# Kernel optimization log

Measured on AMD Instinct MI355X. Metric: run time of the kernel, lower is better.

## Reference

```python
import jax, jax.numpy as jnp
import numpy as np

NUM_HEADS = 16
KEY_DIM = 64
B, S, D = 2, 2048, 1024


def setup_inputs() -> dict:
    key = jax.random.key(0)
    ks = jax.random.split(key, 5)
    scale = 1.0 / np.sqrt(D)
    return {
        "x": jax.random.normal(ks[0], (B, S, D), dtype=jnp.float32),
        "Wq": jax.random.normal(ks[1], (D, NUM_HEADS * KEY_DIM), dtype=jnp.float32) * scale,
        "Wk": jax.random.normal(ks[2], (D, NUM_HEADS * KEY_DIM), dtype=jnp.float32) * scale,
        "Wv": jax.random.normal(ks[3], (D, NUM_HEADS * KEY_DIM), dtype=jnp.float32) * scale,
        "Wo": jax.random.normal(ks[4], (NUM_HEADS * KEY_DIM, D), dtype=jnp.float32) * scale,
    }


def reference(x, Wq, Wk, Wv, Wo):
    b, s, d = x.shape
    h, kd = NUM_HEADS, KEY_DIM
    # QKV projections -> [B, H, S, Kd]
    q = (x @ Wq).reshape(b, s, h, kd).transpose(0, 2, 1, 3)
    k = (x @ Wk).reshape(b, s, h, kd).transpose(0, 2, 1, 3)
    v = (x @ Wv).reshape(b, s, h, kd).transpose(0, 2, 1, 3)
    # scaled dot-product attention, full [B,H,S,S] scores (faithful to source)
    logits = jnp.einsum("bhqd,bhkd->bhqk", q, k) / jnp.sqrt(jnp.float32(kd))
    attn = jax.nn.softmax(logits, axis=-1)
    out = jnp.einsum("bhqk,bhkd->bhqd", attn, v)  # [B,H,S,Kd]
    out = out.transpose(0, 2, 1, 3).reshape(b, s, h * kd)
    return out @ Wo
```

## Files before the change

kernel.cpp:

```cpp
#include <hip/hip_runtime.h>


typedef __attribute__((ext_vector_type(8))) short short8;
typedef __attribute__((ext_vector_type(4))) float f32x4;

#define M_ROWS 4096
#define N_COLS 1024
#define K_DIM  1024
#define SEQ    2048

#define QSCALE 0.18033688011111772f

#if defined(__has_builtin)
#if __has_builtin(__builtin_amdgcn_exp2f)
#define EXP2(x) __builtin_amdgcn_exp2f(x)
#endif
#endif
#ifndef EXP2
#define EXP2(x) exp2f(x)
#endif

#define WAITCNT_VM8 0x0F78

__device__ inline unsigned short f2bf(float f) {
  unsigned int u = __float_as_uint(f);
  u += 0x7fffu + ((u >> 16) & 1u);
  return (unsigned short)(u >> 16);
}

__device__ inline unsigned int pack2bf(float a, float b) {
  unsigned int ua = __float_as_uint(a); ua += 0x7fffu + ((ua >> 16) & 1u);
  unsigned int ub = __float_as_uint(b); ub += 0x7fffu + ((ub >> 16) & 1u);
  return (ua >> 16) | (ub & 0xffff0000u);
}

__device__ inline void async_load16(const unsigned short* gptr, unsigned short* lptr) {
  __builtin_amdgcn_global_load_lds(
      (const __attribute__((address_space(1))) unsigned int*)gptr,
      (__attribute__((address_space(3))) unsigned int*)lptr, 16, 0, 0);
}

__global__ void detect_kernel(const unsigned short* __restrict__ x, int* __restrict__ flag) {
  __shared__ int bad;
  if (threadIdx.x == 0) bad = 0;
  __syncthreads();
  for (int i = threadIdx.x; i < 1024; i += 256) {
    float f = __uint_as_float((unsigned int)x[i] << 16);
    float a = fabsf(f);
    if (!(a < 1e4f)) atomicOr(&bad, 1);
  }
  __syncthreads();
  if (threadIdx.x == 0) *flag = bad ? 0 : 1;
}

__global__ void convert_kernel(const void* __restrict__ src, unsigned short* __restrict__ dst,
                               int n4, const int* __restrict__ flag) {
  const int isbf = *flag;
  const int stride = gridDim.x * blockDim.x;
  for (int i = blockIdx.x * blockDim.x + threadIdx.x; i < n4; i += stride) {
    if (isbf) {
      ((uint2*)dst)[i] = ((const uint2*)src)[i];
    } else {
      float4 v = ((const float4*)src)[i];
      ushort4 o;
      o.x = f2bf(v.x); o.y = f2bf(v.y); o.z = f2bf(v.z); o.w = f2bf(v.w);
      ((ushort4*)dst)[i] = o;
    }
  }
}

__global__ __launch_bounds__(256) void convert_wT4_kernel(
    const void* __restrict__ s0, const void* __restrict__ s1,
    const void* __restrict__ s2, const void* __restrict__ s3,
    unsigned short* __restrict__ d0, unsigned short* __restrict__ d1,
    unsigned short* __restrict__ d2, unsigned short* __restrict__ d3,
    const int* __restrict__ flag) {
  __shared__ unsigned short t[32][33];
  const int z = blockIdx.z;
  const void* src = (z == 0) ? s0 : (z == 1) ? s1 : (z == 2) ? s2 : s3;
  unsigned short* dst = (z == 0) ? d0 : (z == 1) ? d1 : (z == 2) ? d2 : d3;
  const int tid = threadIdx.x;
  const int r0 = blockIdx.y * 32, c0 = blockIdx.x * 32;
  const int kr = tid >> 3, nc = (tid & 7) * 4;
  if (*flag) {
    const unsigned short* W = (const unsigned short*)src;
    uint2 v = *(const uint2*)(W + (size_t)(r0 + kr) * K_DIM + c0 + nc);
    t[kr][nc] = v.x & 0xffff; t[kr][nc + 1] = v.x >> 16;
    t[kr][nc + 2] = v.y & 0xffff; t[kr][nc + 3] = v.y >> 16;
  } else {
    const float* W = (const float*)src;
    float4 v = *(const float4*)(W + (size_t)(r0 + kr) * K_DIM + c0 + nc);
    t[kr][nc] = f2bf(v.x); t[kr][nc + 1] = f2bf(v.y);
    t[kr][nc + 2] = f2bf(v.z); t[kr][nc + 3] = f2bf(v.w);
  }
  __syncthreads();
  const int nr = tid >> 3, kc = (tid & 7) * 4;
  uint2 w;
  w.x = (unsigned int)t[kc][nr] | ((unsigned int)t[kc + 1][nr] << 16);
  w.y = (unsigned int)t[kc + 2][nr] | ((unsigned int)t[kc + 3][nr] << 16);
  *(uint2*)(dst + (size_t)(c0 + nr) * K_DIM + r0 + kc) = w;
}

#define GEMM_MAIN_LOOP(Aptr, Bptr, KTOT)                                          \
  f32x4 acc[4][4];                                                                \
  _Pragma("unroll") for (int i = 0; i < 4; ++i)                                   \
  _Pragma("unroll") for (int j = 0; j < 4; ++j)                                   \
      acc[i][j] = (f32x4){0.f, 0.f, 0.f, 0.f};                                    \
  for (int kb = 0; kb < (KTOT); kb += 64) {                                       \
    _Pragma("unroll") for (int r = 0; r < 4; ++r) {                               \
      int s = r * 256 + wave * 64 + lane;                                         \
      int row = s >> 3, c = s & 7;                                                \
      int g = c ^ (row & 7);                                                      \
      async_load16((Aptr) + (size_t)(m0 + row) * (KTOT) + kb + g * 8,             \
                   &As[(size_t)(r * 256 + wave * 64) * 8]);                       \
      async_load16((Bptr) + (size_t)(n0 + row) * (KTOT) + kb + g * 8,             \
                   &Bs[(size_t)(r * 256 + wave * 64) * 8]);                       \
    }                                                                             \
    __syncthreads();                                                              \
    _Pragma("unroll") for (int h = 0; h < 2; ++h) {                               \
      short8 am[4], bn[4];                                                        \
      _Pragma("unroll") for (int i = 0; i < 4; ++i) {                             \
        int row = wr * 64 + i * 16 + l15;                                         \
        int cc = (h * 4 + quad) ^ (row & 7);                                      \
        am[i] = *(const short8*)(&As[row * 64 + cc * 8]);                         \
      }                                                                           \
      _Pragma("unroll") for (int j = 0; j < 4; ++j) {                             \
        int row = wc * 64 + j * 16 + l15;                                         \
        int cc = (h * 4 + quad) ^ (row & 7);                                      \
        bn[j] = *(const short8*)(&Bs[row * 64 + cc * 8]);                         \
      }                                                                           \
      _Pragma("unroll") for (int i = 0; i < 4; ++i)                               \
      _Pragma("unroll") for (int j = 0; j < 4; ++j)                               \
          acc[i][j] = __builtin_amdgcn_mfma_f32_16x16x32_bf16(am[i], bn[j],       \
                                                              acc[i][j], 0, 0, 0);\
    }                                                                             \
    __syncthreads();                                                              \
  }

__global__ __launch_bounds__(256) void qkv_gemm_kernel(
    const unsigned short* __restrict__ Xb,
    const unsigned short* __restrict__ Wqt,
    const unsigned short* __restrict__ Wkt,
    const unsigned short* __restrict__ Wvt,
    unsigned short* __restrict__ Qb,
    unsigned short* __restrict__ Kb,
    unsigned short* __restrict__ Vt) {
  __shared__ __align__(16) unsigned short As[128 * 64];
  __shared__ __align__(16) unsigned short Bs[128 * 64];
  const int tid = threadIdx.x;
  const int wave = tid >> 6, lane = tid & 63;
  const int quad = lane >> 4, l15 = lane & 15;
  const int wr = wave >> 1, wc = wave & 1;
  const int m0 = blockIdx.x * 128;
  const int n0 = blockIdx.y * 128;
  const int wsel = blockIdx.z;
  const unsigned short* __restrict__ Bt =
      (wsel == 0) ? Wqt : ((wsel == 1) ? Wkt : Wvt);

  GEMM_MAIN_LOOP(Xb, Bt, K_DIM)

#pragma unroll
  for (int i = 0; i < 4; ++i) {
#pragma unroll
    for (int j = 0; j < 4; ++j) {
      int mbase = m0 + wr * 64 + i * 16 + quad * 4;
      int n = n0 + wc * 64 + j * 16 + l15;
      int h = n >> 6, d = n & 63;
      if (wsel == 2) {
        int b_ = mbase >> 11, s = mbase & 2047;
        uint2 w;
        w.x = pack2bf(acc[i][j][0], acc[i][j][1]);
        w.y = pack2bf(acc[i][j][2], acc[i][j][3]);
        *(uint2*)(Vt + ((size_t)(b_ * 16 + h) * 64 + d) * SEQ + s) = w;
      } else {
#pragma unroll
        for (int r = 0; r < 4; ++r) {
          int m = mbase + r;
          int b_ = m >> 11, s = m & 2047;
          float val = acc[i][j][r];
          if (wsel == 0)
            Qb[((size_t)(b_ * 16 + h) * SEQ + s) * 64 + d] = f2bf(val * QSCALE);
          else
            Kb[((size_t)(b_ * 16 + h) * SEQ + s) * 64 + d] = f2bf(val);
        }
      }
    }
  }
}

__global__ __launch_bounds__(256, 2) void flash_kernel(
    const unsigned short* __restrict__ Qb,
    const unsigned short* __restrict__ Kb,
    const unsigned short* __restrict__ Vt,
    unsigned short* __restrict__ Ob) {
  __shared__ __align__(16) unsigned short Klds[2][128 * 64];
  __shared__ __align__(16) unsigned short Vlds[2][64 * 128];
  __shared__ __align__(16) unsigned short Plds[4][16 * 128];
  const int tid = threadIdx.x;
  const int wave = tid >> 6, lane = tid & 63;
  const int quad = lane >> 4, l15 = lane & 15;
  const int bh = blockIdx.y;
  const int qbase = blockIdx.x * 128 + wave * 32;

  const unsigned short* __restrict__ Qp = Qb + (size_t)bh * SEQ * 64;
  const unsigned short* __restrict__ Kp = Kb + (size_t)bh * SEQ * 64;
  const unsigned short* __restrict__ Vp = Vt + (size_t)bh * 64 * SEQ;

  short8 qf[2][2];
#pragma unroll
  for (int g = 0; g < 2; ++g)
#pragma unroll
    for (int h = 0; h < 2; ++h)
      qf[g][h] = *(const short8*)(Qp + (size_t)(qbase + g * 16 + l15) * 64 + h * 32 + quad * 8);

  f32x4 O[2][4];
#pragma unroll
  for (int g = 0; g < 2; ++g)
#pragma unroll
    for (int t = 0; t < 4; ++t) O[g][t] = (f32x4){0.f, 0.f, 0.f, 0.f};
  float l_i[2] = {0.f, 0.f};

#define FLASH_DMA(KB, BUF)                                                     \
  _Pragma("unroll") for (int r = 0; r < 4; ++r) {                              \
    int s = r * 256 + tid;                                                     \
    int krow = s >> 3, kc = s & 7;                                             \
    int kg = kc ^ (krow & 7);                                                  \
    async_load16(Kp + (size_t)((KB) + krow) * 64 + kg * 8,                     \
                 &Klds[BUF][(size_t)(r * 256 + wave * 64) * 8]);               \
    int vrow = s >> 4, vc = s & 15;                                            \
    int vg = vc ^ (vrow & 15);                                                 \
    async_load16(Vp + (size_t)vrow * SEQ + (KB) + vg * 8,                      \
                 &Vlds[BUF][(size_t)(r * 256 + wave * 64) * 8]);               \
  }

  FLASH_DMA(0, 0)

  for (int kb = 0; kb < SEQ; kb += 128) {
    const int p = (kb >> 7) & 1;
    const int kbn = (kb + 128) & (SEQ - 1);
    FLASH_DMA(kbn, p ^ 1)
    __builtin_amdgcn_s_waitcnt(WAITCNT_VM8);
    __syncthreads();

    f32x4 sT[2][8];
#pragma unroll
    for (int t = 0; t < 8; ++t) {
      int row = t * 16 + l15;
      int c0 = quad ^ (row & 7), c1 = (quad + 4) ^ (row & 7);
      short8 k0 = *(const short8*)(&Klds[p][row * 64 + c0 * 8]);
      short8 k1 = *(const short8*)(&Klds[p][row * 64 + c1 * 8]);
      sT[0][t] = __builtin_amdgcn_mfma_f32_16x16x32_bf16(k0, qf[0][0],
                 (f32x4){0.f, 0.f, 0.f, 0.f}, 0, 0, 0);
      sT[0][t] = __builtin_amdgcn_mfma_f32_16x16x32_bf16(k1, qf[0][1], sT[0][t], 0, 0, 0);
      sT[1][t] = __builtin_amdgcn_mfma_f32_16x16x32_bf16(k0, qf[1][0],
                 (f32x4){0.f, 0.f, 0.f, 0.f}, 0, 0, 0);
      sT[1][t] = __builtin_amdgcn_mfma_f32_16x16x32_bf16(k1, qf[1][1], sT[1][t], 0, 0, 0);
    }

    short8 pb[2][4];
#pragma unroll
    for (int g = 0; g < 2; ++g) {
      float rs = 0.f;
#pragma unroll
      for (int t = 0; t < 8; ++t) {
        float p0 = EXP2(sT[g][t][0]);
        float p1 = EXP2(sT[g][t][1]);
        float p2 = EXP2(sT[g][t][2]);
        float p3 = EXP2(sT[g][t][3]);
        sT[g][t][0] = p0; sT[g][t][1] = p1; sT[g][t][2] = p2; sT[g][t][3] = p3;
        rs += (p0 + p1) + (p2 + p3);
      }
      rs += __shfl_xor(rs, 16);
      rs += __shfl_xor(rs, 32);
      l_i[g] += rs;

#pragma unroll
      for (int t = 0; t < 8; ++t) {
        uint2 w; w.x = pack2bf(sT[g][t][0], sT[g][t][1]);
        w.y = pack2bf(sT[g][t][2], sT[g][t][3]);
        *(uint2*)(&Plds[wave][l15 * 128 + (((2 * t + (quad >> 1)) ^ l15) * 8)
                             + (quad & 1) * 4]) = w;
      }
#pragma unroll
      for (int m = 0; m < 4; ++m)
        pb[g][m] = *(const short8*)(&Plds[wave][l15 * 128 + (((m * 4 + quad) ^ l15) * 8)]);
    }

#pragma unroll
    for (int td = 0; td < 4; ++td) {
      int row = td * 16 + l15;
#pragma unroll
      for (int m = 0; m < 4; ++m) {
        short8 vf = *(const short8*)(&Vlds[p][row * 128 + (((m * 4 + quad) ^ l15) * 8)]);
        O[0][td] = __builtin_amdgcn_mfma_f32_16x16x32_bf16(vf, pb[0][m], O[0][td], 0, 0, 0);
        O[1][td] = __builtin_amdgcn_mfma_f32_16x16x32_bf16(vf, pb[1][m], O[1][td], 0, 0, 0);
      }
    }
    __syncthreads();
  }

  const int b_ = bh >> 4, h = bh & 15;
#pragma unroll
  for (int g = 0; g < 2; ++g) {
    const float inv = 1.f / l_i[g];
    unsigned short* orow = Ob + ((size_t)(b_ * SEQ) + qbase + g * 16 + l15) * N_COLS + h * 64;
#pragma unroll
    for (int t = 0; t < 4; ++t) {
      uint2 w;
      w.x = pack2bf(O[g][t][0] * inv, O[g][t][1] * inv);
      w.y = pack2bf(O[g][t][2] * inv, O[g][t][3] * inv);
      *(uint2*)(orow + t * 16 + quad * 4) = w;
    }
  }
#undef FLASH_DMA
}

__global__ __launch_bounds__(256) void out_gemm_kernel(
    const unsigned short* __restrict__ Ob,
    const unsigned short* __restrict__ Wot,
    void* __restrict__ out,
    const int* __restrict__ flag) {
  __shared__ __align__(16) unsigned short As[128 * 64];
  __shared__ __align__(16) unsigned short Bs[128 * 64];
  const int tid = threadIdx.x;
  const int wave = tid >> 6, lane = tid & 63;
  const int quad = lane >> 4, l15 = lane & 15;
  const int wr = wave >> 1, wc = wave & 1;
  const int m0 = blockIdx.x * 128;
  const int n0 = blockIdx.y * 128;
  const int isbf = *flag;

  GEMM_MAIN_LOOP(Ob, Wot, N_COLS)

#pragma unroll
  for (int i = 0; i < 4; ++i) {
#pragma unroll
    for (int j = 0; j < 4; ++j) {
      int mbase = m0 + wr * 64 + i * 16 + quad * 4;
      int n = n0 + wc * 64 + j * 16 + l15;
#pragma unroll
      for (int r = 0; r < 4; ++r) {
        float val = acc[i][j][r];
        if (isbf) ((unsigned short*)out)[(size_t)(mbase + r) * K_DIM + n] = f2bf(val);
        else      ((float*)out)[(size_t)(mbase + r) * K_DIM + n] = val;
      }
    }
  }
}

extern "C" void kernel_launch(void* const* d_in, const int* in_sizes, int n_in,
                              void* d_out, int out_size, void* d_ws, size_t ws_size,
                              hipStream_t stream) {
  const void* x  = d_in[0];
  const void* wq = d_in[1];
  const void* wk = d_in[2];
  const void* wv = d_in[3];
  const void* wo = d_in[4];

  char* ws = (char*)d_ws;
  size_t off = 0;
  int* flag = (int*)(ws + off);                 off += 256;
  unsigned short* xb  = (unsigned short*)(ws + off); off += (size_t)M_ROWS * K_DIM * 2;
  unsigned short* wqt = (unsigned short*)(ws + off); off += (size_t)K_DIM * N_COLS * 2;
  unsigned short* wkt = (unsigned short*)(ws + off); off += (size_t)K_DIM * N_COLS * 2;
  unsigned short* wvt = (unsigned short*)(ws + off); off += (size_t)K_DIM * N_COLS * 2;
  unsigned short* wot = (unsigned short*)(ws + off); off += (size_t)N_COLS * K_DIM * 2;
  unsigned short* Qb  = (unsigned short*)(ws + off); off += (size_t)M_ROWS * 1024 * 2;
  unsigned short* Kb  = (unsigned short*)(ws + off); off += (size_t)M_ROWS * 1024 * 2;
  unsigned short* Vtb = (unsigned short*)(ws + off); off += (size_t)M_ROWS * 1024 * 2;
  unsigned short* Ob  = (unsigned short*)(ws + off); off += (size_t)M_ROWS * N_COLS * 2;
  (void)ws_size; (void)in_sizes; (void)n_in; (void)out_size;

  detect_kernel<<<1, 256, 0, stream>>>((const unsigned short*)x, flag);

  convert_kernel<<<2048, 256, 0, stream>>>(x, xb, (M_ROWS * K_DIM) / 4, flag);
  convert_wT4_kernel<<<dim3(32, 32, 4), 256, 0, stream>>>(wq, wk, wv, wo,
                                                          wqt, wkt, wvt, wot, flag);

  qkv_gemm_kernel<<<dim3(32, 8, 3), 256, 0, stream>>>(xb, wqt, wkt, wvt, Qb, Kb, Vtb);
  flash_kernel<<<dim3(16, 32), 256, 0, stream>>>(Qb, Kb, Vtb, Ob);
  out_gemm_kernel<<<dim3(32, 8), 256, 0, stream>>>(Ob, wot, d_out, flag);
}
```

Measured before the change: 208.0 us.

## Double-buffer GEMM LDS tiles with K-step 32 and async prefetch

The QKV and output projection GEMMs now load the next 32-wide K slice into a second LDS buffer while MFMAs run on the current one. A partial vmcnt wait replaces the old load-then-sync-then-compute sequence, and the swizzle is adapted to 4-chunk rows. Launch bounds request 3 blocks per CU. The goal is to hide global-to-LDS latency. In exchange it issues twice as many barriers per unit of K, and the loop's last iteration fetches a wrapped-around tile it never uses.

```diff
diff --git a/kernel.cpp b/kernel.cpp
--- a/kernel.cpp
+++ b/kernel.cpp
@@ -21,6 +21,7 @@
 #endif
 
 #define WAITCNT_VM8 0x0F78
+#define WAITCNT_VM4 0x0F74
 
 __device__ inline unsigned short f2bf(float f) {
   unsigned int u = __float_as_uint(f);
@@ -101,43 +102,46 @@
   *(uint2*)(dst + (size_t)(c0 + nr) * K_DIM + r0 + kc) = w;
 }
 
+#define GEMM_DMA(Aptr, Bptr, KTOT, KB, BUF)                                       \
+  _Pragma("unroll") for (int r = 0; r < 2; ++r) {                                 \
+    int s = r * 256 + wave * 64 + lane;                                           \
+    int row = s >> 2, c = s & 3;                                                  \
+    int g = c ^ ((row ^ (row >> 2)) & 3);                                         \
+    async_load16((Aptr) + (size_t)(m0 + row) * (KTOT) + (KB) + g * 8,             \
+                 &As[BUF][(size_t)(r * 256 + wave * 64) * 8]);                    \
+    async_load16((Bptr) + (size_t)(n0 + row) * (KTOT) + (KB) + g * 8,             \
+                 &Bs[BUF][(size_t)(r * 256 + wave * 64) * 8]);                    \
+  }
+
 #define GEMM_MAIN_LOOP(Aptr, Bptr, KTOT)                                          \
   f32x4 acc[4][4];                                                                \
   _Pragma("unroll") for (int i = 0; i < 4; ++i)                                   \
   _Pragma("unroll") for (int j = 0; j < 4; ++j)                                   \
       acc[i][j] = (f32x4){0.f, 0.f, 0.f, 0.f};                                    \
-  for (int kb = 0; kb < (KTOT); kb += 64) {                                       \
-    _Pragma("unroll") for (int r = 0; r < 4; ++r) {                               \
-      int s = r * 256 + wave * 64 + lane;                                         \
-      int row = s >> 3, c = s & 7;                                                \
-      int g = c ^ (row & 7);                                                      \
-      async_load16((Aptr) + (size_t)(m0 + row) * (KTOT) + kb + g * 8,             \
-                   &As[(size_t)(r * 256 + wave * 64) * 8]);                       \
-      async_load16((Bptr) + (size_t)(n0 + row) * (KTOT) + kb + g * 8,             \
-                   &Bs[(size_t)(r * 256 + wave * 64) * 8]);                       \
+  const int xr = (l15 ^ (l15 >> 2)) & 3;                                          \
+  GEMM_DMA(Aptr, Bptr, KTOT, 0, 0)                                                \
+  for (int kb = 0; kb < (KTOT); kb += 32) {                                       \
+    const int pp = (kb >> 5) & 1;                                                 \
+    const int kbn = (kb + 32) & ((KTOT) - 1);                                     \
+    GEMM_DMA(Aptr, Bptr, KTOT, kbn, pp ^ 1)                                       \
+    __builtin_amdgcn_s_waitcnt(WAITCNT_VM4);                                      \
+    __syncthreads();                                                              \
+    short8 am[4], bn[4];                                                          \
+    _Pragma("unroll") for (int i = 0; i < 4; ++i) {                               \
+      int arow = wr * 64 + i * 16 + l15;                                          \
+      int brow = wc * 64 + i * 16 + l15;                                          \
+      int cc = quad ^ xr;                                                         \
+      am[i] = *(const short8*)(&As[pp][arow * 32 + cc * 8]);                      \
+      bn[i] = *(const short8*)(&Bs[pp][brow * 32 + cc * 8]);                      \
     }                                                                             \
+    _Pragma("unroll") for (int i = 0; i < 4; ++i)                                 \
+    _Pragma("unroll") for (int j = 0; j < 4; ++j)                                 \
+        acc[i][j] = __builtin_amdgcn_mfma_f32_16x16x32_bf16(am[i], bn[j],         \
+                                                            acc[i][j], 0, 0, 0); \
     __syncthreads();                                                              \
-    _Pragma("unroll") for (int h = 0; h < 2; ++h) {                               \
-      short8 am[4], bn[4];                                                        \
-      _Pragma("unroll") for (int i = 0; i < 4; ++i) {                             \
-        int row = wr * 64 + i * 16 + l15;                                         \
-        int cc = (h * 4 + quad) ^ (row & 7);                                      \
-        am[i] = *(const short8*)(&As[row * 64 + cc * 8]);                         \
-      }                                                                           \
-      _Pragma("unroll") for (int j = 0; j < 4; ++j) {                             \
-        int row = wc * 64 + j * 16 + l15;                                         \
-        int cc = (h * 4 + quad) ^ (row & 7);                                      \
-        bn[j] = *(const short8*)(&Bs[row * 64 + cc * 8]);                         \
-      }                                                                           \
-      _Pragma("unroll") for (int i = 0; i < 4; ++i)                               \
-      _Pragma("unroll") for (int j = 0; j < 4; ++j)                               \
-          acc[i][j] = __builtin_amdgcn_mfma_f32_16x16x32_bf16(am[i], bn[j],       \
-                                                              acc[i][j], 0, 0, 0);\
-    }                                                                             \
-    __syncthreads();                                                              \
-  }
-
-__global__ __launch_bounds__(256) void qkv_gemm_kernel(
+  }
+
+__global__ __launch_bounds__(256, 3) void qkv_gemm_kernel(
     const unsigned short* __restrict__ Xb,
     const unsigned short* __restrict__ Wqt,
     const unsigned short* __restrict__ Wkt,
@@ -145,8 +149,8 @@
     unsigned short* __restrict__ Qb,
     unsigned short* __restrict__ Kb,
     unsigned short* __restrict__ Vt) {
-  __shared__ __align__(16) unsigned short As[128 * 64];
-  __shared__ __align__(16) unsigned short Bs[128 * 64];
+  __shared__ __align__(16) unsigned short As[2][128 * 32];
+  __shared__ __align__(16) unsigned short Bs[2][128 * 32];
   const int tid = threadIdx.x;
   const int wave = tid >> 6, lane = tid & 63;
   const int quad = lane >> 4, l15 = lane & 15;
@@ -315,13 +319,13 @@
 #undef FLASH_DMA
 }
 
-__global__ __launch_bounds__(256) void out_gemm_kernel(
+__global__ __launch_bounds__(256, 3) void out_gemm_kernel(
     const unsigned short* __restrict__ Ob,
     const unsigned short* __restrict__ Wot,
     void* __restrict__ out,
     const int* __restrict__ flag) {
-  __shared__ __align__(16) unsigned short As[128 * 64];
-  __shared__ __align__(16) unsigned short Bs[128 * 64];
+  __shared__ __align__(16) unsigned short As[2][128 * 32];
+  __shared__ __align__(16) unsigned short Bs[2][128 * 32];
   const int tid = threadIdx.x;
   const int wave = tid >> 6, lane = tid & 63;
   const int quad = lane >> 4, l15 = lane & 15;
```

Result: faster. 200.8 us (-3.5%).
